# Kernel tuning notes

Hardware: AMD Instinct MI355X
Metric: run time of the kernel (lower is better)

Reference implementation:

```python
import jax, jax.numpy as jnp
import numpy as np

N = 100000      # num_nodes
E = 1600000     # num_edges
F_IN = 5        # in_features
H = 64          # hidden_channels
HC = H // 2     # classifier hidden
L = 3           # num GCN layers
EPS = 1e-5      # BatchNorm eps


def setup_inputs() -> dict:
    key = jax.random.key(0)
    ks = jax.random.split(key, 12)
    s = 0.1
    return {
        "x": jax.random.normal(ks[0], (N, F_IN), dtype=jnp.float32),
        "edge_index": jax.random.randint(ks[1], (2, E), 0, N, dtype=jnp.int32),
        "W_in": jax.random.normal(ks[2], (F_IN, H), dtype=jnp.float32) * s,
        "b_in": jax.random.normal(ks[3], (H,), dtype=jnp.float32) * s,
        "conv_W": jax.random.normal(ks[4], (L, H, H), dtype=jnp.float32) * s,
        "conv_b": jax.random.normal(ks[5], (L, H), dtype=jnp.float32) * s,
        "bn_gamma": jnp.ones((L, H), dtype=jnp.float32),
        "bn_beta": jnp.zeros((L, H), dtype=jnp.float32),
        "W1": jax.random.normal(ks[6], (H, HC), dtype=jnp.float32) * s,
        "b1": jax.random.normal(ks[7], (HC,), dtype=jnp.float32) * s,
        "W2": jax.random.normal(ks[8], (HC, 1), dtype=jnp.float32) * s,
        "b2": jax.random.normal(ks[9], (1,), dtype=jnp.float32) * s,
    }


def reference(x, edge_index, W_in, b_in, conv_W, conv_b, bn_gamma, bn_beta, W1, b1, W2, b2):
    src, dst = edge_index[0], edge_index[1]

    # input projection + ReLU
    h = jax.nn.relu(x @ W_in + b_in)  # (N, H)

    # GCN symmetric normalization with self-loops (PyG GCNConv default):
    # deg includes the self-loop weight of 1.
    deg = jax.ops.segment_sum(jnp.ones((E,), dtype=h.dtype), dst, num_segments=N) + 1.0
    dinv = jax.lax.rsqrt(deg)                       # deg^{-1/2}, (N,)
    edge_coef = dinv[src] * dinv[dst]               # (E,)
    self_coef = dinv * dinv                         # (N,)

    for i in range(L):
        hw = h @ conv_W[i]                          # linear (no bias yet), (N, H)
        # gather -> scale -> scatter-add aggregation, plus self-loop term
        agg = jax.ops.segment_sum(hw[src] * edge_coef[:, None], dst, num_segments=N)
        agg = agg + hw * self_coef[:, None] + conv_b[i]
        # BatchNorm1d over nodes (batch statistics; eval dropout = identity)
        mean = jnp.mean(agg, axis=0)
        var = jnp.var(agg, axis=0)
        h = bn_gamma[i] * (agg - mean) * jax.lax.rsqrt(var + EPS) + bn_beta[i]
        h = jax.nn.relu(h)

    # classifier MLP: H -> H//2 -> 1, squeeze to (N,)
    logits = (jax.nn.relu(h @ W1 + b1) @ W2 + b2).squeeze(-1)
    return logits
```

## Files before the change

kernel.cpp:

```cpp
#include <hip/hip_runtime.h>

#define NN 100000
#define EE 1600000
#define EPSV 1e-5f
#define QW 12500
#define HN 50000

using short8 = __attribute__((ext_vector_type(8))) short;
using floatx4 = __attribute__((ext_vector_type(4))) float;

__device__ __forceinline__ unsigned short f2bf(float f) {
    union { float f; unsigned int u; } cv;
    cv.f = f;
    unsigned int u = cv.u;
    u += 0x7FFFu + ((u >> 16) & 1u);
    return (unsigned short)(u >> 16);
}

__device__ __forceinline__ float bf2f(unsigned short u) {
    union { unsigned int i; float f; } cv;
    cv.i = ((unsigned int)u) << 16;
    return cv.f;
}

__global__ void deg_kernel(const int* __restrict__ dst, int* __restrict__ degi8) {
    int e = blockIdx.x * 256 + threadIdx.x;
    if (e >= EE) return;
    int q = blockIdx.x & 7;
    atomicAdd(&degi8[q * NN + dst[e]], 1);
}

__global__ void scan1(const int* __restrict__ degi8, int* __restrict__ degi,
                      int* __restrict__ offsets, int* __restrict__ partial,
                      float* __restrict__ dinv) {
    __shared__ int sdata[256];
    int t = threadIdx.x;
    int n = blockIdx.x * 256 + t;
    int v = 0;
    if (n < NN) {
#pragma unroll
        for (int q = 0; q < 8; ++q) v += degi8[q * NN + n];
        degi[n] = v;
        dinv[n] = rsqrtf((float)v + 1.0f);
    }
    sdata[t] = v;
    __syncthreads();
    for (int off = 1; off < 256; off <<= 1) {
        int x = (t >= off) ? sdata[t - off] : 0;
        __syncthreads();
        sdata[t] += x;
        __syncthreads();
    }
    if (n < NN) offsets[n] = sdata[t] - v;
    if (t == 255) partial[blockIdx.x] = sdata[255];
}

__global__ void scan2(int* __restrict__ partial, int* __restrict__ partial_pref,
                      int nparts, float* __restrict__ stats) {
    __shared__ int sdata[512];
    int t = threadIdx.x;
    if (t < 384) stats[t] = 0.f;
    int v = (t < nparts) ? partial[t] : 0;
    sdata[t] = v;
    __syncthreads();
    for (int off = 1; off < 512; off <<= 1) {
        int x = (t >= off) ? sdata[t - off] : 0;
        __syncthreads();
        sdata[t] += x;
        __syncthreads();
    }
    if (t < nparts) partial_pref[t] = sdata[t] - v;
}

__global__ void fill_kernel(const int* __restrict__ src, const int* __restrict__ dst,
                            int* __restrict__ offsets,
                            const int* __restrict__ partial_pref,
                            const float* __restrict__ dinv,
                            int2* __restrict__ sorted) {
    int q = blockIdx.x & 7;
    int e = (blockIdx.x >> 3) * 256 + threadIdx.x;
    if (e >= EE) return;
    int d = dst[e];
    if ((unsigned)(d - q * QW) >= (unsigned)QW) return;
    int s = src[e];
    int idx = partial_pref[d >> 8] + atomicAdd(&offsets[d], 1);
    int2 rec;
    rec.x = s;
    rec.y = __float_as_int(dinv[s] * dinv[d]);
    sorted[idx] = rec;
}

__global__ __launch_bounds__(256) void gemm64_bn(const float* __restrict__ in,
                                                 const float* __restrict__ x,
                                                 const float* __restrict__ Win,
                                                 const float* __restrict__ bin,
                                                 const float* __restrict__ stats,
                                                 const float* __restrict__ gamma,
                                                 const float* __restrict__ beta,
                                                 const float* __restrict__ W,
                                                 unsigned short* __restrict__ out,
                                                 int mode) {
    __shared__ __align__(16) unsigned short As[64 * 72];
    __shared__ __align__(16) unsigned short Wt[64 * 72];
    __shared__ float scale[64], shift[64];
    __shared__ float Wins[320];
    __shared__ float bins[64];
    int t = threadIdx.x;
    if (mode == 1) {
        if (t < 64) {
            const float invN = 1.0f / (float)NN;
            float mean = stats[t] * invN;
            float var = stats[64 + t] * invN - mean * mean;
            float rstd = rsqrtf(var + EPSV);
            float sc = gamma[t] * rstd;
            scale[t] = sc;
            shift[t] = beta[t] - mean * sc;
        }
    } else {
        for (int i = t; i < 320; i += 256) Wins[i] = Win[i];
        if (t < 64) bins[t] = bin[t];
    }
    for (int i = t; i < 4096; i += 256) {
        int k = i >> 6, c = i & 63;
        Wt[c * 72 + k] = f2bf(W[k * 64 + c]);
    }
    __syncthreads();
    int base = blockIdx.x * 64;
    if (mode == 1) {
        for (int i = t; i < 4096; i += 256) {
            int r = i >> 6, c = i & 63;
            float v = 0.f;
            if (base + r < NN) {
                v = in[(base + r) * 64 + c];
                v = fmaxf(v * scale[c] + shift[c], 0.f);
            }
            As[r * 72 + c] = f2bf(v);
        }
    } else {
        for (int i = t; i < 4096; i += 256) {
            int r = i >> 6, c = i & 63;
            int n = base + r;
            float v = 0.f;
            if (n < NN) {
                float acc = bins[c];
#pragma unroll
                for (int k = 0; k < 5; ++k) acc += x[n * 5 + k] * Wins[k * 64 + c];
                v = fmaxf(acc, 0.f);
            }
            As[r * 72 + c] = f2bf(v);
        }
    }
    __syncthreads();
    int wv = t >> 6;
    int lane = t & 63;
    int quad = lane >> 4;
    int mm = lane & 15;
    short8 a0 = *(const short8*)&As[(wv * 16 + mm) * 72 + quad * 8];
    short8 a1 = *(const short8*)&As[(wv * 16 + mm) * 72 + 32 + quad * 8];
#pragma unroll
    for (int ct = 0; ct < 4; ++ct) {
        short8 b0 = *(const short8*)&Wt[(ct * 16 + mm) * 72 + quad * 8];
        short8 b1 = *(const short8*)&Wt[(ct * 16 + mm) * 72 + 32 + quad * 8];
        floatx4 acc = {0.f, 0.f, 0.f, 0.f};
        acc = __builtin_amdgcn_mfma_f32_16x16x32_bf16(a0, b0, acc, 0, 0, 0);
        acc = __builtin_amdgcn_mfma_f32_16x16x32_bf16(a1, b1, acc, 0, 0, 0);
#pragma unroll
        for (int reg = 0; reg < 4; ++reg) {
            int n = base + wv * 16 + quad * 4 + reg;
            if (n < NN) out[(ct * NN + n) * 16 + mm] = f2bf(acc[reg]);
        }
    }
}

__global__ __launch_bounds__(256) void agg_kernel(const unsigned int* __restrict__ hw32,
                                                  const int2* __restrict__ sorted,
                                                  const int* __restrict__ offsets,
                                                  const int* __restrict__ partial_pref,
                                                  const int* __restrict__ degi,
                                                  const float* __restrict__ dinv,
                                                  const float* __restrict__ b,
                                                  float* __restrict__ agg,
                                                  float* __restrict__ stats) {
    int t = threadIdx.x;
    int lane = t & 63;
    int w = t >> 6;
    int q = blockIdx.x & 7;
    int g = q & 3;
    int h = q >> 2;
    int bi = blockIdx.x >> 3;
    int cwu = lane & 7;
    int eg = lane >> 3;
    int gbase = g * NN;
    float b0 = b[g * 16 + 2 * cwu], b1v = b[g * 16 + 2 * cwu + 1];
    float bsx = 0.f, bsy = 0.f, bqx = 0.f, bqy = 0.f;
    int n0 = h * HN;
    for (int n = n0 + bi * 4 + w; n < n0 + HN; n += 256 * 4) {
        int cnt = degi[n];
        int start = partial_pref[n >> 8] + offsets[n] - cnt;
        float ax = 0.f, ay = 0.f;
        if (eg == 0) {
            unsigned int u = hw32[(unsigned)(gbase + n) * 8 + cwu];
            float di = dinv[n];
            float sc = di * di;
            ax = bf2f((unsigned short)(u & 0xffffu)) * sc + b0;
            ay = bf2f((unsigned short)(u >> 16)) * sc + b1v;
        }
        for (int base = 0; base < cnt; base += 16) {
            int e0 = base + eg, e1 = base + 8 + eg;
            long long rr0 = 0, rr1 = 0;
            if (e0 < cnt) rr0 = __builtin_nontemporal_load((const long long*)&sorted[start + e0]);
            if (e1 < cnt) rr1 = __builtin_nontemporal_load((const long long*)&sorted[start + e1]);
            int s0 = (int)(unsigned int)(rr0 & 0xffffffffLL);
            int s1 = (int)(unsigned int)(rr1 & 0xffffffffLL);
            unsigned int u0 = hw32[(unsigned)(gbase + s0) * 8 + cwu];
            unsigned int u1 = hw32[(unsigned)(gbase + s1) * 8 + cwu];
            float c0 = __int_as_float((int)(rr0 >> 32));
            float c1 = __int_as_float((int)(rr1 >> 32));
            ax += bf2f((unsigned short)(u0 & 0xffffu)) * c0;
            ay += bf2f((unsigned short)(u0 >> 16)) * c0;
            ax += bf2f((unsigned short)(u1 & 0xffffu)) * c1;
            ay += bf2f((unsigned short)(u1 >> 16)) * c1;
        }
        ax += __shfl_xor(ax, 8);
        ay += __shfl_xor(ay, 8);
        ax += __shfl_xor(ax, 16);
        ay += __shfl_xor(ay, 16);
        ax += __shfl_xor(ax, 32);
        ay += __shfl_xor(ay, 32);
        if (eg == 0) {
            unsigned long long pv =
                ((unsigned long long)__float_as_uint(ay) << 32) | __float_as_uint(ax);
            __builtin_nontemporal_store(pv,
                (unsigned long long*)&agg[n * 64 + g * 16 + 2 * cwu]);
            bsx += ax;
            bsy += ay;
            bqx += ax * ax;
            bqy += ay * ay;
        }
    }
    __shared__ float red[2][4][16];
    if (eg == 0) {
        red[0][w][2 * cwu] = bsx;
        red[0][w][2 * cwu + 1] = bsy;
        red[1][w][2 * cwu] = bqx;
        red[1][w][2 * cwu + 1] = bqy;
    }
    __syncthreads();
    if (w == 0 && lane < 16) {
        float s = red[0][0][lane] + red[0][1][lane] + red[0][2][lane] + red[0][3][lane];
        float ss = red[1][0][lane] + red[1][1][lane] + red[1][2][lane] + red[1][3][lane];
        atomicAdd(&stats[g * 16 + lane], s);
        atomicAdd(&stats[64 + g * 16 + lane], ss);
    }
}

__global__ __launch_bounds__(256) void classifier(const float* __restrict__ agg,
                                                  const float* __restrict__ stats,
                                                  const float* __restrict__ gamma,
                                                  const float* __restrict__ beta,
                                                  const float* __restrict__ W1,
                                                  const float* __restrict__ b1,
                                                  const float* __restrict__ W2,
                                                  const float* __restrict__ b2,
                                                  float* __restrict__ out) {
    __shared__ float W1s[2048];
    __shared__ float b1s[32];
    __shared__ float W2s[32];
    __shared__ float scale[64], shift[64];
    int t = threadIdx.x;
    for (int i = t; i < 2048; i += 256) W1s[i] = W1[i];
    if (t < 32) {
        b1s[t] = b1[t];
        W2s[t] = W2[t];
    }
    if (t < 64) {
        const float invN = 1.0f / (float)NN;
        float mean = stats[t] * invN;
        float var = stats[64 + t] * invN - mean * mean;
        float rstd = rsqrtf(var + EPSV);
        float sc = gamma[t] * rstd;
        scale[t] = sc;
        shift[t] = beta[t] - mean * sc;
    }
    __syncthreads();
    int n = blockIdx.x * 256 + t;
    if (n >= NN) return;
    float4 h4[16];
    const float4* hp = (const float4*)(agg + n * 64);
#pragma unroll
    for (int i = 0; i < 16; ++i) h4[i] = hp[i];
    float* hr = (float*)h4;
#pragma unroll
    for (int k = 0; k < 64; ++k) hr[k] = fmaxf(hr[k] * scale[k] + shift[k], 0.f);
    float o = b2[0];
    for (int c = 0; c < 32; ++c) {
        float z = b1s[c];
#pragma unroll
        for (int k = 0; k < 64; ++k) z += hr[k] * W1s[k * 32 + c];
        o += fmaxf(z, 0.f) * W2s[c];
    }
    out[n] = o;
}

extern "C" void kernel_launch(void* const* d_in, const int* in_sizes, int n_in,
                              void* d_out, int out_size, void* d_ws, size_t ws_size,
                              hipStream_t stream) {
    const float* x    = (const float*)d_in[0];
    const int*   ei   = (const int*)d_in[1];
    const float* Win  = (const float*)d_in[2];
    const float* bin  = (const float*)d_in[3];
    const float* cW   = (const float*)d_in[4];
    const float* cb   = (const float*)d_in[5];
    const float* gam  = (const float*)d_in[6];
    const float* bet  = (const float*)d_in[7];
    const float* W1   = (const float*)d_in[8];
    const float* b1   = (const float*)d_in[9];
    const float* W2   = (const float*)d_in[10];
    const float* b2   = (const float*)d_in[11];
    float* out = (float*)d_out;

    unsigned short* hw = (unsigned short*)d_ws;
    float* agg   = (float*)d_ws + NN * 32;
    float* dinv  = agg + NN * 64;
    float* stats = dinv + NN;
    int*  degi        = (int*)(stats + 3 * 128);
    int*  offsets     = degi + NN;
    int2* sorted      = (int2*)(offsets + NN);
    int*  partial     = (int*)(sorted + EE);
    int*  partial_pref = partial + 512;
    int*  degi8       = partial_pref + 512;

    const int* src = ei;
    const int* dst = ei + EE;

    const int NB = (NN + 255) / 256;
    const int EB = (EE + 255) / 256;

    (void)hipMemsetAsync(degi8, 0, 8 * NN * sizeof(int), stream);

    deg_kernel<<<EB, 256, 0, stream>>>(dst, degi8);
    scan1<<<NB, 256, 0, stream>>>(degi8, degi, offsets, partial, dinv);
    scan2<<<1, 512, 0, stream>>>(partial, partial_pref, NB, stats);
    fill_kernel<<<EB * 8, 256, 0, stream>>>(src, dst, offsets, partial_pref, dinv, sorted);

    for (int i = 0; i < 3; ++i) {
        gemm64_bn<<<(NN + 63) / 64, 256, 0, stream>>>(
            agg, x, Win, bin, stats + (i - 1) * 128, gam + (i - 1) * 64,
            bet + (i - 1) * 64, cW + i * 4096, hw, i > 0 ? 1 : 0);
        agg_kernel<<<2048, 256, 0, stream>>>((const unsigned int*)hw, sorted, offsets,
                                             partial_pref, degi, dinv, cb + i * 64, agg,
                                             stats + i * 128);
    }

    classifier<<<(NN + 255) / 256, 256, 0, stream>>>(agg, stats + 2 * 128, gam + 2 * 64,
                                                     bet + 2 * 64, W1, b1, W2, b2, out);
}
```

Before: 634.9 us.

## Load edge records once per wavefront and broadcast via shuffles; simplify fill

The aggregation loop now has each lane load one sorted edge record per 64-edge chunk and broadcasts source index and coefficient through wavefront shuffles. Before, every 8-lane group reloaded the same record, so this cuts redundant record loads. The fill kernel drops its 8-way partitioning of destination ranges, which had launched eight passes over the edge list, and now does a single pass with scattered writes. The agg store also becomes a plain float2 store instead of a nontemporal one, and the extra shuffles add ALU and latency per edge.

```diff
diff --git a/kernel.cpp b/kernel.cpp
--- a/kernel.cpp
+++ b/kernel.cpp
@@ -3,7 +3,6 @@
 #define NN 100000
 #define EE 1600000
 #define EPSV 1e-5f
-#define QW 12500
 #define HN 50000
 
 using short8 = __attribute__((ext_vector_type(8))) short;
@@ -77,11 +76,9 @@
                             const int* __restrict__ partial_pref,
                             const float* __restrict__ dinv,
                             int2* __restrict__ sorted) {
-    int q = blockIdx.x & 7;
-    int e = (blockIdx.x >> 3) * 256 + threadIdx.x;
+    int e = blockIdx.x * 256 + threadIdx.x;
     if (e >= EE) return;
     int d = dst[e];
-    if ((unsigned)(d - q * QW) >= (unsigned)QW) return;
     int s = src[e];
     int idx = partial_pref[d >> 8] + atomicAdd(&offsets[d], 1);
     int2 rec;
@@ -188,38 +185,40 @@
     int g = q & 3;
     int h = q >> 2;
     int bi = blockIdx.x >> 3;
-    int cwu = lane & 7;
     int eg = lane >> 3;
-    int gbase = g * NN;
-    float b0 = b[g * 16 + 2 * cwu], b1v = b[g * 16 + 2 * cwu + 1];
+    int cu = lane & 7;
+    unsigned gb = (unsigned)g * NN;
+    float b0 = b[g * 16 + 2 * cu], b1v = b[g * 16 + 2 * cu + 1];
     float bsx = 0.f, bsy = 0.f, bqx = 0.f, bqy = 0.f;
-    int n0 = h * HN;
-    for (int n = n0 + bi * 4 + w; n < n0 + HN; n += 256 * 4) {
+    int slot = bi * 4 + w;
+    int nend = h * HN + HN;
+    for (int n = h * HN + slot; n < nend; n += 1024) {
         int cnt = degi[n];
         int start = partial_pref[n >> 8] + offsets[n] - cnt;
         float ax = 0.f, ay = 0.f;
         if (eg == 0) {
-            unsigned int u = hw32[(unsigned)(gbase + n) * 8 + cwu];
+            unsigned int u = hw32[(gb + (unsigned)n) * 8 + cu];
             float di = dinv[n];
             float sc = di * di;
             ax = bf2f((unsigned short)(u & 0xffffu)) * sc + b0;
             ay = bf2f((unsigned short)(u >> 16)) * sc + b1v;
         }
-        for (int base = 0; base < cnt; base += 16) {
-            int e0 = base + eg, e1 = base + 8 + eg;
-            long long rr0 = 0, rr1 = 0;
-            if (e0 < cnt) rr0 = __builtin_nontemporal_load((const long long*)&sorted[start + e0]);
-            if (e1 < cnt) rr1 = __builtin_nontemporal_load((const long long*)&sorted[start + e1]);
-            int s0 = (int)(unsigned int)(rr0 & 0xffffffffLL);
-            int s1 = (int)(unsigned int)(rr1 & 0xffffffffLL);
-            unsigned int u0 = hw32[(unsigned)(gbase + s0) * 8 + cwu];
-            unsigned int u1 = hw32[(unsigned)(gbase + s1) * 8 + cwu];
-            float c0 = __int_as_float((int)(rr0 >> 32));
-            float c1 = __int_as_float((int)(rr1 >> 32));
-            ax += bf2f((unsigned short)(u0 & 0xffffu)) * c0;
-            ay += bf2f((unsigned short)(u0 >> 16)) * c0;
-            ax += bf2f((unsigned short)(u1 & 0xffffu)) * c1;
-            ay += bf2f((unsigned short)(u1 >> 16)) * c1;
+        for (int base = 0; base < cnt; base += 64) {
+            int m = min(64, cnt - base);
+            int2 rec = make_int2(0, 0);
+            if (lane < m) rec = sorted[start + base + lane];
+            for (int k = 0; k < m; k += 16) {
+                int s0 = __shfl(rec.x, k + eg);
+                int s1 = __shfl(rec.x, k + 8 + eg);
+                unsigned int u0 = hw32[(gb + (unsigned)s0) * 8 + cu];
+                unsigned int u1 = hw32[(gb + (unsigned)s1) * 8 + cu];
+                float c0 = __int_as_float(__shfl(rec.y, k + eg));
+                float c1 = __int_as_float(__shfl(rec.y, k + 8 + eg));
+                ax += bf2f((unsigned short)(u0 & 0xffffu)) * c0;
+                ay += bf2f((unsigned short)(u0 >> 16)) * c0;
+                ax += bf2f((unsigned short)(u1 & 0xffffu)) * c1;
+                ay += bf2f((unsigned short)(u1 >> 16)) * c1;
+            }
         }
         ax += __shfl_xor(ax, 8);
         ay += __shfl_xor(ay, 8);
@@ -228,10 +227,7 @@
         ax += __shfl_xor(ax, 32);
         ay += __shfl_xor(ay, 32);
         if (eg == 0) {
-            unsigned long long pv =
-                ((unsigned long long)__float_as_uint(ay) << 32) | __float_as_uint(ax);
-            __builtin_nontemporal_store(pv,
-                (unsigned long long*)&agg[n * 64 + g * 16 + 2 * cwu]);
+            *(float2*)&agg[(unsigned)n * 64 + g * 16 + 2 * cu] = make_float2(ax, ay);
             bsx += ax;
             bsy += ay;
             bqx += ax * ax;
@@ -240,10 +236,10 @@
     }
     __shared__ float red[2][4][16];
     if (eg == 0) {
-        red[0][w][2 * cwu] = bsx;
-        red[0][w][2 * cwu + 1] = bsy;
-        red[1][w][2 * cwu] = bqx;
-        red[1][w][2 * cwu + 1] = bqy;
+        red[0][w][2 * cu] = bsx;
+        red[0][w][2 * cu + 1] = bsy;
+        red[1][w][2 * cu] = bqx;
+        red[1][w][2 * cu + 1] = bqy;
     }
     __syncthreads();
     if (w == 0 && lane < 16) {
@@ -341,7 +337,7 @@
     deg_kernel<<<EB, 256, 0, stream>>>(dst, degi8);
     scan1<<<NB, 256, 0, stream>>>(degi8, degi, offsets, partial, dinv);
     scan2<<<1, 512, 0, stream>>>(partial, partial_pref, NB, stats);
-    fill_kernel<<<EB * 8, 256, 0, stream>>>(src, dst, offsets, partial_pref, dinv, sorted);
+    fill_kernel<<<EB, 256, 0, stream>>>(src, dst, offsets, partial_pref, dinv, sorted);
 
     for (int i = 0; i < 3; ++i) {
         gemm64_bn<<<(NN + 63) / 64, 256, 0, stream>>>(
```

Measured after the change: 525.3 us. 17.3% less time.
